# Kernel optimization log

Measured on AMD Instinct MI355X. Metric: run time of the kernel, lower is better.

Reference implementation:

```python
import jax, jax.numpy as jnp
import numpy as np

TAU = 2.0       # LIF time constant
VTH = 1.0       # V_THRESHOLD
ALPHA = 2.0     # ATan surrogate alpha (spikingjelly default)
SCALE = 0.125

@jax.custom_vjp
def spike(x):
    # Heaviside spike with ATan surrogate gradient
    return (x >= 0.0).astype(x.dtype)

def _spike_fwd(x):
    return (x >= 0.0).astype(x.dtype), x

def _spike_bwd(x, g):
    sg = (ALPHA / 2.0) / (1.0 + (jnp.pi / 2.0 * ALPHA * x) ** 2)
    return (g * sg,)

spike.defvjp(_spike_fwd, _spike_bwd)

def lif(x_seq):
    # multi-step LIF: v += (x - v)/tau; spike; hard reset (v_reset=0, detach_reset)
    def step(v, x):
        v = v + (x - v) / TAU
        s = spike(v - VTH)
        v = v * (1.0 - jax.lax.stop_gradient(s))
        return v, s
    _, s = jax.lax.scan(step, jnp.zeros_like(x_seq[0]), x_seq)
    return s

def conn_lif(x_seq, y_seq):
    # connecting LIF: membrane charged by conv output + identity shortcut
    def step(v, xy):
        x, y = xy
        v = v + ((x + y) - v) / TAU
        s = spike(v - VTH)
        v = v * (1.0 - jax.lax.stop_gradient(s))
        return v, s
    _, s = jax.lax.scan(step, jnp.zeros_like(x_seq[0]), (x_seq, y_seq))
    return s

def conv1x1(x, W, b):
    # x: [T,B,C,N]; 1x1 Conv1d == channel GEMM
    return jnp.einsum('tbcn,oc->tbon', x, W) + b[None, None, :, None]

def setup_inputs() -> dict:
    key = jax.random.key(0)
    T, B, C, H, W = 4, 16, 512, 32, 32
    ks = jax.random.split(key, 5)
    wscale = 1.0 / np.sqrt(C)
    inp = {
        'x': jax.random.normal(ks[0], (T, B, C, H, W), jnp.float32),
        'Wq': jax.random.normal(ks[1], (C, C), jnp.float32) * wscale,
        'bq': jnp.zeros((C,), jnp.float32),
        'Wk': jax.random.normal(ks[2], (C, C), jnp.float32) * wscale,
        'bk': jnp.zeros((C,), jnp.float32),
        'Wv': jax.random.normal(ks[3], (C, C), jnp.float32) * wscale,
        'bv': jnp.zeros((C,), jnp.float32),
        'Wp': jax.random.normal(ks[4], (C, C), jnp.float32) * wscale,
        'bp': jnp.zeros((C,), jnp.float32),
        'num_heads': 8,
    }
    return inp

def reference(x, Wq, bq, Wk, bk, Wv, bv, Wp, bp, num_heads):
    T, B, C, H, W = x.shape
    N = H * W
    h = num_heads
    d = C // h
    qkv_x = x.reshape(T, B, C, N)

    def to_heads(s):  # [T,B,C,N] -> [T,B,h,N,d]
        return s.reshape(T, B, h, d, N).transpose(0, 1, 2, 4, 3)

    q = to_heads(lif(conv1x1(qkv_x, Wq, bq)))
    k = to_heads(lif(conv1x1(qkv_x, Wk, bk)))
    v = to_heads(lif(conv1x1(qkv_x, Wv, bv)))

    kv = jnp.einsum('tbhnd,tbhne->tbhde', k, v)            # K^T V: [T,B,h,d,d]
    out = jnp.einsum('tbhnd,tbhde->tbhne', q, kv) * SCALE  # Q @ (K^T V)
    out = out.transpose(0, 1, 2, 4, 3).reshape(T, B, C, N)
    out = lif(out)                                          # attn_sn
    out = conv1x1(out, Wp, bp).reshape(T, B, C, H, W)       # proj_reparam
    out = conn_lif(out, x)                                  # proj_sn(out, x)
    return out
```

## Files before the change

kernel.cpp:

```cpp
#include <hip/hip_runtime.h>

#define T_ 4
#define B_ 16
#define C_ 512
#define N_ 1024
#define H_ 8
#define D_ 64
#define SPK_ELEMS (33554432ull)

typedef _Float16 half8v __attribute__((ext_vector_type(8)));
typedef _Float16 half4v __attribute__((ext_vector_type(4)));
typedef float f32x4 __attribute__((ext_vector_type(4)));

#define KV_OFF_N  100663296ull
#define WB_OFF_N  109051904ull
#define XS_OFF_N  113246208ull

#define QKV_INV_SCALE (1.0f / 8388608.0f)
#define PROJ_INV_SCALE (1.0f / 4096.0f)

#define GLD16(gp, loff) \
  __builtin_amdgcn_global_load_lds( \
      (const __attribute__((address_space(1))) void*)(gp), \
      (__attribute__((address_space(3))) void*)(lds + (loff)), 16, 0, 0)

__global__ __launch_bounds__(256) void convert_w(
    const float* __restrict__ w0, const float* __restrict__ w1,
    const float* __restrict__ w2, const float* __restrict__ w3,
    _Float16* __restrict__ wb)
{
  int idx = blockIdx.x * 256 + threadIdx.x;
  int p = idx >> 18, rem = idx & 262143;
  const float* src = (p == 0) ? w0 : (p == 1) ? w1 : (p == 2) ? w2 : w3;
  float v = src[rem] * 4096.0f;
  _Float16 h1 = (_Float16)v;
  float r1 = v - (float)h1;
  _Float16 h2 = (_Float16)r1;
  size_t base = ((size_t)(p * 2)) << 18;
  wb[base + rem] = h1;
  wb[base + 262144 + rem] = h2;
}

__global__ __launch_bounds__(256) void convert_x(
    const float* __restrict__ x, _Float16* __restrict__ xs)
{
  __shared__ float tile[32][33];
  const int tb = blockIdx.z;
  const int c0 = blockIdx.y * 32, n0 = blockIdx.x * 32;
  const int tx = threadIdx.x, ty = threadIdx.y;
  const float* src = x + ((size_t)tb * C_ + c0) * N_ + n0;
#pragma unroll
  for (int k = 0; k < 4; ++k)
    tile[ty + 8 * k][tx] = src[(size_t)(ty + 8 * k) * N_ + tx];
  __syncthreads();
#pragma unroll
  for (int k = 0; k < 4; ++k) {
    int r = ty + 8 * k;
    float v = tile[tx][r] * 2048.0f;
    _Float16 h1 = (_Float16)v;
    float r1 = v - (float)h1;
    _Float16 h2 = (_Float16)r1;
    size_t o = ((size_t)tb * N_ + n0 + r) * C_ + c0 + tx;
    xs[o] = h1;
    xs[o + 33554432ull] = h2;
  }
}

__global__ __launch_bounds__(512) void qkv_mfma(
    const _Float16* __restrict__ wb, const _Float16* __restrict__ xs,
    const float* __restrict__ bq, const float* __restrict__ bk,
    const float* __restrict__ bv, unsigned char* __restrict__ spikes_base)
{
  __shared__ __align__(16) char lds[81920];
  const int tid = threadIdx.x;
  const int lane = tid & 63, wave = tid >> 6;
  const int ln15 = lane & 15, lq = lane >> 4;
  const int wr = wave & 3, wn = wave >> 2;

  const int l = blockIdx.x + 12 * blockIdx.y + 384 * blockIdx.z;
  const int xcd = l & 7, slot = l >> 3;
  const int g = (slot / 12) * 8 + xcd;
  const int m = slot % 12;
  const int ot = m & 3, p = m >> 2;
  const int ntb = g & 31, b = g >> 5;
  const int o0 = ot * 128, n0 = ntb * 32;

#define WB_(k) (((k) & 1) * 16384)
#define XB_(k) (32768 + ((k) % 3) * 16384)

  const _Float16* gw[2];
#pragma unroll
  for (int i = 0; i < 2; ++i) {
    int u = i * 512 + tid;
    int s = u >> 9, rem = u & 511;
    int row = rem >> 2, pc = rem & 3;
    int lc = pc ^ ((row >> 1) & 3);
    gw[i] = wb + (((size_t)(p * 2 + s)) << 18) + (size_t)(o0 + row) * C_ + lc * 8;
  }
  const _Float16* gx[2];
#pragma unroll
  for (int i = 0; i < 2; ++i) {
    int v = i * 512 + tid;
    int s = v >> 9, rem = v & 511;
    int t = rem >> 7, rem2 = rem & 127;
    int row = rem2 >> 2, pc = rem2 & 3;
    int lc = pc ^ ((row >> 1) & 3);
    gx[i] = xs + ((size_t)s * 33554432ull) +
            ((size_t)((t * B_ + b) * N_ + n0 + row)) * C_ + lc * 8;
  }
  const int sb = (tid & 448) * 16;

  f32x4 acc[T_][2];
#pragma unroll
  for (int t = 0; t < T_; ++t)
#pragma unroll
    for (int mt = 0; mt < 2; ++mt)
      acc[t][mt] = (f32x4){0.f, 0.f, 0.f, 0.f};

  int offA[2][2], offB[2];
#pragma unroll
  for (int s = 0; s < 2; ++s) {
#pragma unroll
    for (int mt = 0; mt < 2; ++mt) {
      int r = wr * 32 + mt * 16 + ln15;
      offA[s][mt] = s * 8192 + r * 64 + ((lq ^ ((r >> 1) & 3)) << 4);
    }
    {
      int n = wn * 16 + ln15;
      offB[s] = s * 8192 + n * 64 + ((lq ^ ((n >> 1) & 3)) << 4);
    }
  }

  auto compute = [&](int wbase, int xbase) {
    half8v wa[2][2];
#pragma unroll
    for (int s = 0; s < 2; ++s)
#pragma unroll
      for (int mt = 0; mt < 2; ++mt)
        wa[s][mt] = *(const half8v*)&lds[wbase + offA[s][mt]];

    __builtin_amdgcn_s_setprio(1);
#pragma unroll
    for (int t = 0; t < T_; ++t) {
      half8v xb[2];
#pragma unroll
      for (int s = 0; s < 2; ++s)
        xb[s] = *(const half8v*)&lds[xbase + offB[s] + t * 2048];
#pragma unroll
      for (int mt = 0; mt < 2; ++mt) {
        f32x4 a = acc[t][mt];
        a = __builtin_amdgcn_mfma_f32_16x16x32_f16(wa[0][mt], xb[1], a, 0, 0, 0);
        a = __builtin_amdgcn_mfma_f32_16x16x32_f16(wa[1][mt], xb[0], a, 0, 0, 0);
        a = __builtin_amdgcn_mfma_f32_16x16x32_f16(wa[0][mt], xb[0], a, 0, 0, 0);
        acc[t][mt] = a;
      }
    }
    __builtin_amdgcn_s_setprio(0);
  };

#pragma unroll
  for (int i = 0; i < 2; ++i)
    GLD16(gx[i], XB_(0) + i * 8192 + sb);
#pragma unroll
  for (int i = 0; i < 2; ++i) gx[i] += 32;
#pragma unroll
  for (int i = 0; i < 2; ++i)
    GLD16(gw[i], WB_(0) + i * 8192 + sb);
#pragma unroll
  for (int i = 0; i < 2; ++i) gw[i] += 32;
#pragma unroll
  for (int i = 0; i < 2; ++i)
    GLD16(gx[i], XB_(1) + i * 8192 + sb);
#pragma unroll
  for (int i = 0; i < 2; ++i) gx[i] += 32;
  asm volatile("s_waitcnt vmcnt(2)" ::: "memory");
  __builtin_amdgcn_s_barrier();
  __builtin_amdgcn_sched_barrier(0);

#pragma unroll
  for (int kk = 0; kk < 16; ++kk) {
    if (kk < 15) {
#pragma unroll
      for (int i = 0; i < 2; ++i)
        GLD16(gw[i], WB_(kk + 1) + i * 8192 + sb);
#pragma unroll
      for (int i = 0; i < 2; ++i) gw[i] += 32;
    }
    if (kk < 14) {
#pragma unroll
      for (int i = 0; i < 2; ++i)
        GLD16(gx[i], XB_(kk + 2) + i * 8192 + sb);
#pragma unroll
      for (int i = 0; i < 2; ++i) gx[i] += 32;
    }
    __builtin_amdgcn_sched_barrier(0);

    compute(WB_(kk), XB_(kk));

    if (kk < 15) {
      __builtin_amdgcn_sched_barrier(0);
      if (kk < 14) asm volatile("s_waitcnt vmcnt(2)" ::: "memory");
      else         asm volatile("s_waitcnt vmcnt(0)" ::: "memory");
      __builtin_amdgcn_s_barrier();
      __builtin_amdgcn_sched_barrier(0);
    }
  }

#undef WB_
#undef XB_

  const float* bias = (p == 0) ? bq : (p == 1) ? bk : bv;
  const int n = n0 + wn * 16 + ln15;
  if (p == 0) {
    unsigned char* spq = spikes_base;
#pragma unroll
    for (int mt = 0; mt < 2; ++mt) {
      int obase = o0 + wr * 32 + mt * 16 + lq * 4;
      float b4[4] = {bias[obase], bias[obase + 1], bias[obase + 2], bias[obase + 3]};
      float vm[4] = {0.f, 0.f, 0.f, 0.f};
#pragma unroll
      for (int t = 0; t < T_; ++t) {
        unsigned char sj[4];
#pragma unroll
        for (int r = 0; r < 4; ++r) {
          float y = acc[t][mt][r] * QKV_INV_SCALE + b4[r];
          float v = vm[r] + (y - vm[r]) * 0.5f;
          bool s = (v >= 1.0f);
          sj[r] = s ? 1 : 0;
          vm[r] = s ? 0.f : v;
        }
        *(uchar4*)&spq[((size_t)(t * B_ + b) * N_ + n) * C_ + obase] =
            make_uchar4(sj[0], sj[1], sj[2], sj[3]);
      }
    }
  } else {
    unsigned char* sp = spikes_base + (size_t)p * SPK_ELEMS;
#pragma unroll
    for (int mt = 0; mt < 2; ++mt)
#pragma unroll
      for (int r = 0; r < 4; ++r) {
        int o = o0 + wr * 32 + mt * 16 + lq * 4 + r;
        float bo = bias[o];
        float vmem = 0.f;
#pragma unroll
        for (int t = 0; t < T_; ++t) {
          float y = acc[t][mt][r] * QKV_INV_SCALE + bo;
          float v = vmem + (y - vmem) * 0.5f;
          bool s = (v >= 1.0f);
          sp[((size_t)(t * B_ + b) * C_ + o) * N_ + n] = s ? 1 : 0;
          vmem = s ? 0.f : v;
        }
      }
  }
}

__global__ __launch_bounds__(256) void kv_f16(
    const unsigned char* __restrict__ sk, const unsigned char* __restrict__ sv,
    float* __restrict__ kvout)
{
  __shared__ _Float16 Kf[64 * 264];
  __shared__ _Float16 Vf[64 * 264];
  const int tid = threadIdx.x;
  const int lane = tid & 63, wave = tid >> 6;
  const int ln15 = lane & 15, lq = lane >> 4;
  const int h = blockIdx.x, b = blockIdx.y, t = blockIdx.z;

  const unsigned char* kb = sk + ((size_t)(t * B_ + b) * C_ + h * D_) * N_;
  const unsigned char* vb = sv + ((size_t)(t * B_ + b) * C_ + h * D_) * N_;

  f32x4 acc[4];
#pragma unroll
  for (int et = 0; et < 4; ++et) acc[et] = (f32x4){0.f, 0.f, 0.f, 0.f};

  const int row = tid >> 2, seg = (tid & 3) * 64;

  for (int nc = 0; nc < N_; nc += 256) {
    const unsigned char* kr = kb + (size_t)row * N_ + nc + seg;
    const unsigned char* vr = vb + (size_t)row * N_ + nc + seg;
#pragma unroll
    for (int j = 0; j < 16; ++j) {
      unsigned wk = *(const unsigned*)(kr + j * 4);
      unsigned lo = ((wk & 0xFFu) | ((wk & 0xFF00u) << 8)) * 0x3C00u;
      unsigned hi = (((wk >> 16) & 0xFFu) | ((wk >> 8) & 0xFF0000u)) * 0x3C00u;
      *(uint2*)&Kf[row * 264 + seg + j * 4] = make_uint2(lo, hi);
      unsigned wv = *(const unsigned*)(vr + j * 4);
      unsigned lo2 = ((wv & 0xFFu) | ((wv & 0xFF00u) << 8)) * 0x3C00u;
      unsigned hi2 = (((wv >> 16) & 0xFFu) | ((wv >> 8) & 0xFF0000u)) * 0x3C00u;
      *(uint2*)&Vf[row * 264 + seg + j * 4] = make_uint2(lo2, hi2);
    }
    __syncthreads();
#pragma unroll
    for (int ks = 0; ks < 8; ++ks) {
      half8v a = *(const half8v*)&Kf[(wave * 16 + ln15) * 264 + ks * 32 + lq * 8];
#pragma unroll
      for (int et = 0; et < 4; ++et) {
        half8v bf = *(const half8v*)&Vf[(et * 16 + ln15) * 264 + ks * 32 + lq * 8];
        acc[et] = __builtin_amdgcn_mfma_f32_16x16x32_f16(a, bf, acc[et], 0, 0, 0);
      }
    }
    __syncthreads();
  }

  float* o = kvout + ((size_t)(t * B_ + b) * H_ + h) * (D_ * D_);
#pragma unroll
  for (int et = 0; et < 4; ++et)
#pragma unroll
    for (int r = 0; r < 4; ++r) {
      int d = wave * 16 + lq * 4 + r;
      int e = et * 16 + ln15;
      o[d * D_ + e] = acc[et][r];
    }
}

__global__ __launch_bounds__(256) void attn_mfma(
    const unsigned char* __restrict__ sq2, const float* __restrict__ kv,
    unsigned short* __restrict__ sa)
{
  __shared__ _Float16 Qs[128 * 72];
  __shared__ _Float16 KVT[64 * 72];
  const int tid = threadIdx.x;
  const int lane = tid & 63, wave = tid >> 6;
  const int ln15 = lane & 15, lq = lane >> 4;
  const int n0 = blockIdx.x * 128;
  const int h = blockIdx.y, b = blockIdx.z;

  f32x4 vm[8];
#pragma unroll
  for (int nt = 0; nt < 8; ++nt) vm[nt] = (f32x4){0.f, 0.f, 0.f, 0.f};

  for (int t = 0; t < T_; ++t) {
    __syncthreads();
    const float* kvb = kv + ((size_t)(t * B_ + b) * H_ + h) * (D_ * D_);
#pragma unroll
    for (int l = 0; l < 16; ++l) {
      int idx = l * 256 + tid;
      int e = idx & 63, d = idx >> 6;
      KVT[e * 72 + d] = (_Float16)kvb[d * 64 + e];
    }
    const unsigned char* qb = sq2 + ((size_t)(t * B_ + b) * N_ + n0) * C_ + h * D_;
#pragma unroll
    for (int l = 0; l < 8; ++l) {
      int idx = l * 256 + tid;
      int n = idx >> 4, d4 = (idx & 15) * 4;
      uchar4 qu = *(const uchar4*)&qb[(size_t)n * C_ + d4];
      half4v hv;
      hv.x = qu.x ? (_Float16)1.0f : (_Float16)0.0f;
      hv.y = qu.y ? (_Float16)1.0f : (_Float16)0.0f;
      hv.z = qu.z ? (_Float16)1.0f : (_Float16)0.0f;
      hv.w = qu.w ? (_Float16)1.0f : (_Float16)0.0f;
      *(half4v*)&Qs[n * 72 + d4] = hv;
    }
    __syncthreads();

    half8v af[2];
#pragma unroll
    for (int kk = 0; kk < 2; ++kk)
      af[kk] = *(const half8v*)&KVT[(wave * 16 + ln15) * 72 + kk * 32 + lq * 8];

#pragma unroll
    for (int nt = 0; nt < 8; ++nt) {
      f32x4 a = (f32x4){0.f, 0.f, 0.f, 0.f};
#pragma unroll
      for (int kk = 0; kk < 2; ++kk) {
        half8v bf = *(const half8v*)&Qs[(nt * 16 + ln15) * 72 + kk * 32 + lq * 8];
        a = __builtin_amdgcn_mfma_f32_16x16x32_f16(af[kk], bf, a, 0, 0, 0);
      }
      unsigned short sj[4];
#pragma unroll
      for (int r = 0; r < 4; ++r) {
        float y = a[r] * 0.125f;
        float v = vm[nt][r] + (y - vm[nt][r]) * 0.5f;
        bool s = (v >= 1.0f);
        sj[r] = s ? 0x3C00 : 0;
        vm[nt][r] = s ? 0.f : v;
      }
      int n = n0 + nt * 16 + ln15;
      int c0 = h * D_ + wave * 16 + lq * 4;
      *(ushort4*)&sa[((size_t)(t * B_ + b) * N_ + n) * C_ + c0] =
          make_ushort4(sj[0], sj[1], sj[2], sj[3]);
    }
  }
}

__global__ __launch_bounds__(256) void proj_mfma(
    const _Float16* __restrict__ wb, const _Float16* __restrict__ sa,
    const float* __restrict__ bp, const float* __restrict__ x,
    float* __restrict__ out)
{
  __shared__ __align__(16) char lds[49152];
  const int tid = threadIdx.x;
  const int lane = tid & 63, wave = tid >> 6;
  const int ln15 = lane & 15, lq = lane >> 4;

  const int l = blockIdx.x + 4 * blockIdx.y + 128 * blockIdx.z;
  const int xcd = l & 7, slot = l >> 3;
  const int g = (slot / 4) * 8 + xcd;
  const int ot = slot % 4;
  const int ntb = g & 31, b = g >> 5;
  const int o0 = ot * 128, n0 = ntb * 32;

  const _Float16* gsrc[6];
#pragma unroll
  for (int i = 0; i < 6; ++i) {
    int u = i * 256 + tid;
    if (u < 1024) {
      int s = u >> 9, rem = u & 511;
      int row = rem >> 2, pc = rem & 3;
      int lc = pc ^ ((row >> 1) & 3);
      gsrc[i] = wb + (((size_t)(3 * 2 + s)) << 18) + (size_t)(o0 + row) * C_ + lc * 8;
    } else {
      int v = u - 1024;
      int t = v >> 7, rem2 = v & 127;
      int row = rem2 >> 2, pc = rem2 & 3;
      int lc = pc ^ ((row >> 1) & 3);
      gsrc[i] = sa + ((size_t)((t * B_ + b) * N_ + n0 + row)) * C_ + lc * 8;
    }
  }

  f32x4 acc[T_][2][2];
#pragma unroll
  for (int t = 0; t < T_; ++t)
#pragma unroll
    for (int mt = 0; mt < 2; ++mt)
#pragma unroll
      for (int nt = 0; nt < 2; ++nt)
        acc[t][mt][nt] = (f32x4){0.f, 0.f, 0.f, 0.f};

  int offA[2][2], offB[2];
#pragma unroll
  for (int s = 0; s < 2; ++s)
#pragma unroll
    for (int mt = 0; mt < 2; ++mt) {
      int r = wave * 32 + mt * 16 + ln15;
      offA[s][mt] = s * 8192 + r * 64 + ((lq ^ ((r >> 1) & 3)) << 4);
    }
#pragma unroll
  for (int nt = 0; nt < 2; ++nt) {
    int n = nt * 16 + ln15;
    offB[nt] = 16384 + n * 64 + ((lq ^ ((n >> 1) & 3)) << 4);
  }

  auto compute = [&](int cur) {
    half8v wa[2][2];
#pragma unroll
    for (int s = 0; s < 2; ++s)
#pragma unroll
      for (int mt = 0; mt < 2; ++mt)
        wa[s][mt] = *(const half8v*)&lds[cur + offA[s][mt]];

    __builtin_amdgcn_s_setprio(1);
#pragma unroll
    for (int t = 0; t < T_; ++t) {
      half8v xb[2];
#pragma unroll
      for (int nt = 0; nt < 2; ++nt)
        xb[nt] = *(const half8v*)&lds[cur + offB[nt] + t * 2048];
#pragma unroll
      for (int mt = 0; mt < 2; ++mt)
#pragma unroll
        for (int nt = 0; nt < 2; ++nt) {
          f32x4 a = acc[t][mt][nt];
          a = __builtin_amdgcn_mfma_f32_16x16x32_f16(wa[1][mt], xb[nt], a, 0, 0, 0);
          a = __builtin_amdgcn_mfma_f32_16x16x32_f16(wa[0][mt], xb[nt], a, 0, 0, 0);
          acc[t][mt][nt] = a;
        }
    }
    __builtin_amdgcn_s_setprio(0);
  };

#pragma unroll
  for (int i = 0; i < 6; ++i)
    GLD16(gsrc[i], i * 4096 + (tid & 192) * 16);
#pragma unroll
  for (int i = 0; i < 6; ++i) gsrc[i] += 32;

  for (int kk = 0; kk < 15; ++kk) {
    const int cur = (kk & 1) * 24576;
    const int nxt = 24576 - cur;
#pragma unroll
    for (int i = 0; i < 6; ++i)
      GLD16(gsrc[i], nxt + i * 4096 + (tid & 192) * 16);
#pragma unroll
    for (int i = 0; i < 6; ++i) gsrc[i] += 32;
    __builtin_amdgcn_sched_barrier(0);
    asm volatile("s_waitcnt vmcnt(6)" ::: "memory");
    __builtin_amdgcn_s_barrier();
    __builtin_amdgcn_sched_barrier(0);

    compute(cur);

    asm volatile("s_waitcnt lgkmcnt(0)" ::: "memory");
    __builtin_amdgcn_sched_barrier(0);
    __builtin_amdgcn_s_barrier();
  }
  asm volatile("s_waitcnt vmcnt(0)" ::: "memory");
  __builtin_amdgcn_s_barrier();
  __builtin_amdgcn_sched_barrier(0);
  compute(24576);

#pragma unroll
  for (int mt = 0; mt < 2; ++mt)
#pragma unroll
    for (int r = 0; r < 4; ++r) {
      int o = o0 + wave * 32 + mt * 16 + lq * 4 + r;
      float bo = bp[o];
#pragma unroll
      for (int nt = 0; nt < 2; ++nt) {
        int n = n0 + nt * 16 + ln15;
        float vmem = 0.f;
#pragma unroll
        for (int t = 0; t < T_; ++t) {
          size_t base = ((size_t)(t * B_ + b) * C_ + o) * N_ + n;
          float xv = x[base];
          float pv = acc[t][mt][nt][r] * PROJ_INV_SCALE + bo;
          float v = vmem + ((pv + xv) - vmem) * 0.5f;
          bool s = (v >= 1.0f);
          out[base] = s ? 1.0f : 0.0f;
          vmem = s ? 0.f : v;
        }
      }
    }
}

extern "C" void kernel_launch(void* const* d_in, const int* in_sizes, int n_in,
                              void* d_out, int out_size, void* d_ws, size_t ws_size,
                              hipStream_t stream)
{
  const float* x  = (const float*)d_in[0];
  const float* Wq = (const float*)d_in[1];
  const float* bq = (const float*)d_in[2];
  const float* Wk = (const float*)d_in[3];
  const float* bk = (const float*)d_in[4];
  const float* Wv = (const float*)d_in[5];
  const float* bv = (const float*)d_in[6];
  const float* Wp = (const float*)d_in[7];
  const float* bp = (const float*)d_in[8];
  (void)in_sizes; (void)n_in; (void)out_size; (void)ws_size;

  unsigned char* ws = (unsigned char*)d_ws;
  unsigned char* sq = ws;
  unsigned char* sk = ws + SPK_ELEMS;
  unsigned char* sv = ws + 2 * SPK_ELEMS;
  float* kvbuf = (float*)(ws + KV_OFF_N);
  _Float16* wb = (_Float16*)(ws + WB_OFF_N);
  _Float16* xs = (_Float16*)(ws + XS_OFF_N);
  unsigned short* sa = (unsigned short*)xs;
  float* out = (float*)d_out;

  convert_w<<<4096, 256, 0, stream>>>(Wq, Wk, Wv, Wp, wb);
  convert_x<<<dim3(32, 16, 64), dim3(32, 8), 0, stream>>>(x, xs);
  qkv_mfma<<<dim3(12, 32, 16), 512, 0, stream>>>(wb, xs, bq, bk, bv, ws);
  kv_f16<<<dim3(8, 16, 4), 256, 0, stream>>>(sk, sv, kvbuf);
  attn_mfma<<<dim3(8, 8, 16), 256, 0, stream>>>(sq, kvbuf, sa);
  proj_mfma<<<dim3(4, 32, 16), 256, 0, stream>>>(wb, (const _Float16*)sa, bp, x, out);
}
```

Baseline: 748.2 us.

## Vectorize convert_x transpose and rework proj_mfma into 512-thread triple-buffered pipeline

convert_x now uses 64x64 tiles with float4 global loads and half4 vector stores in place of scalar accesses, which cuts the number of memory transactions in the transpose. proj_mfma moves from 4 to 8 waves per block, giving each wave a 16-column N slice. Weight tiles are now double-buffered and spike tiles triple-buffered, with a prefetch depth of two for spikes. The aim is better latency hiding and higher occupancy in the projection GEMM, at the cost of more LDS per block and more complex wait counts.

```diff
diff --git a/kernel.cpp b/kernel.cpp
--- a/kernel.cpp
+++ b/kernel.cpp
@@ -44,25 +44,42 @@
 __global__ __launch_bounds__(256) void convert_x(
     const float* __restrict__ x, _Float16* __restrict__ xs)
 {
-  __shared__ float tile[32][33];
+  __shared__ float tile[64][65];
   const int tb = blockIdx.z;
-  const int c0 = blockIdx.y * 32, n0 = blockIdx.x * 32;
-  const int tx = threadIdx.x, ty = threadIdx.y;
-  const float* src = x + ((size_t)tb * C_ + c0) * N_ + n0;
-#pragma unroll
-  for (int k = 0; k < 4; ++k)
-    tile[ty + 8 * k][tx] = src[(size_t)(ty + 8 * k) * N_ + tx];
+  const int c0 = blockIdx.y * 64, n0 = blockIdx.x * 64;
+  const int tid = threadIdx.x;
+  {
+    const int tx = tid & 15, ty = tid >> 4;
+    const float* src = x + ((size_t)tb * C_ + c0 + ty) * N_ + n0 + tx * 4;
+#pragma unroll
+    for (int k = 0; k < 4; ++k) {
+      float4 v = *(const float4*)(src + (size_t)(16 * k) * N_);
+      tile[ty + 16 * k][tx * 4 + 0] = v.x;
+      tile[ty + 16 * k][tx * 4 + 1] = v.y;
+      tile[ty + 16 * k][tx * 4 + 2] = v.z;
+      tile[ty + 16 * k][tx * 4 + 3] = v.w;
+    }
+  }
   __syncthreads();
-#pragma unroll
-  for (int k = 0; k < 4; ++k) {
-    int r = ty + 8 * k;
-    float v = tile[tx][r] * 2048.0f;
-    _Float16 h1 = (_Float16)v;
-    float r1 = v - (float)h1;
-    _Float16 h2 = (_Float16)r1;
-    size_t o = ((size_t)tb * N_ + n0 + r) * C_ + c0 + tx;
-    xs[o] = h1;
-    xs[o + 33554432ull] = h2;
+  {
+    const int cg = tid & 15, nl = tid >> 4;
+#pragma unroll
+    for (int k = 0; k < 4; ++k) {
+      int n = nl + 16 * k;
+      half4v d0, d1;
+#pragma unroll
+      for (int j = 0; j < 4; ++j) {
+        float v = tile[cg * 4 + j][n] * 2048.0f;
+        _Float16 h1 = (_Float16)v;
+        float r1 = v - (float)h1;
+        _Float16 h2 = (_Float16)r1;
+        d0[j] = h1;
+        d1[j] = h2;
+      }
+      size_t o = ((size_t)tb * N_ + n0 + n) * C_ + c0 + cg * 4;
+      *(half4v*)&xs[o] = d0;
+      *(half4v*)&xs[o + 33554432ull] = d1;
+    }
   }
 }
 
@@ -382,15 +399,16 @@
   }
 }
 
-__global__ __launch_bounds__(256) void proj_mfma(
+__global__ __launch_bounds__(512) void proj_mfma(
     const _Float16* __restrict__ wb, const _Float16* __restrict__ sa,
     const float* __restrict__ bp, const float* __restrict__ x,
     float* __restrict__ out)
 {
-  __shared__ __align__(16) char lds[49152];
+  __shared__ __align__(16) char lds[57344];
   const int tid = threadIdx.x;
   const int lane = tid & 63, wave = tid >> 6;
   const int ln15 = lane & 15, lq = lane >> 4;
+  const int wr = wave & 3, wn = wave >> 2;
 
   const int l = blockIdx.x + 4 * blockIdx.y + 128 * blockIdx.z;
   const int xcd = l & 7, slot = l >> 3;
@@ -399,125 +417,129 @@
   const int ntb = g & 31, b = g >> 5;
   const int o0 = ot * 128, n0 = ntb * 32;
 
-  const _Float16* gsrc[6];
-#pragma unroll
-  for (int i = 0; i < 6; ++i) {
-    int u = i * 256 + tid;
-    if (u < 1024) {
-      int s = u >> 9, rem = u & 511;
-      int row = rem >> 2, pc = rem & 3;
-      int lc = pc ^ ((row >> 1) & 3);
-      gsrc[i] = wb + (((size_t)(3 * 2 + s)) << 18) + (size_t)(o0 + row) * C_ + lc * 8;
-    } else {
-      int v = u - 1024;
-      int t = v >> 7, rem2 = v & 127;
-      int row = rem2 >> 2, pc = rem2 & 3;
-      int lc = pc ^ ((row >> 1) & 3);
-      gsrc[i] = sa + ((size_t)((t * B_ + b) * N_ + n0 + row)) * C_ + lc * 8;
-    }
-  }
-
-  f32x4 acc[T_][2][2];
+#define WB_(k) (((k) & 1) * 16384)
+#define SB_(k) (32768 + ((k) % 3) * 8192)
+
+  const _Float16* gw[2];
+#pragma unroll
+  for (int i = 0; i < 2; ++i) {
+    int u = i * 512 + tid;
+    int s = u >> 9, rem = u & 511;
+    int row = rem >> 2, pc = rem & 3;
+    int lc = pc ^ ((row >> 1) & 3);
+    gw[i] = wb + (((size_t)(3 * 2 + s)) << 18) + (size_t)(o0 + row) * C_ + lc * 8;
+  }
+  const _Float16* gs;
+  {
+    int t = tid >> 7, rem2 = tid & 127;
+    int row = rem2 >> 2, pc = rem2 & 3;
+    int lc = pc ^ ((row >> 1) & 3);
+    gs = sa + ((size_t)((t * B_ + b) * N_ + n0 + row)) * C_ + lc * 8;
+  }
+  const int sb = (tid & 448) * 16;
+
+  f32x4 acc[T_][2];
 #pragma unroll
   for (int t = 0; t < T_; ++t)
 #pragma unroll
     for (int mt = 0; mt < 2; ++mt)
-#pragma unroll
-      for (int nt = 0; nt < 2; ++nt)
-        acc[t][mt][nt] = (f32x4){0.f, 0.f, 0.f, 0.f};
-
-  int offA[2][2], offB[2];
+      acc[t][mt] = (f32x4){0.f, 0.f, 0.f, 0.f};
+
+  int offA[2][2], offB;
 #pragma unroll
   for (int s = 0; s < 2; ++s)
 #pragma unroll
     for (int mt = 0; mt < 2; ++mt) {
-      int r = wave * 32 + mt * 16 + ln15;
+      int r = wr * 32 + mt * 16 + ln15;
       offA[s][mt] = s * 8192 + r * 64 + ((lq ^ ((r >> 1) & 3)) << 4);
     }
-#pragma unroll
-  for (int nt = 0; nt < 2; ++nt) {
-    int n = nt * 16 + ln15;
-    offB[nt] = 16384 + n * 64 + ((lq ^ ((n >> 1) & 3)) << 4);
-  }
-
-  auto compute = [&](int cur) {
+  {
+    int n = wn * 16 + ln15;
+    offB = n * 64 + ((lq ^ ((n >> 1) & 3)) << 4);
+  }
+
+  auto compute = [&](int wbase, int sbase) {
     half8v wa[2][2];
 #pragma unroll
     for (int s = 0; s < 2; ++s)
 #pragma unroll
       for (int mt = 0; mt < 2; ++mt)
-        wa[s][mt] = *(const half8v*)&lds[cur + offA[s][mt]];
+        wa[s][mt] = *(const half8v*)&lds[wbase + offA[s][mt]];
 
     __builtin_amdgcn_s_setprio(1);
 #pragma unroll
     for (int t = 0; t < T_; ++t) {
-      half8v xb[2];
-#pragma unroll
-      for (int nt = 0; nt < 2; ++nt)
-        xb[nt] = *(const half8v*)&lds[cur + offB[nt] + t * 2048];
-#pragma unroll
-      for (int mt = 0; mt < 2; ++mt)
-#pragma unroll
-        for (int nt = 0; nt < 2; ++nt) {
-          f32x4 a = acc[t][mt][nt];
-          a = __builtin_amdgcn_mfma_f32_16x16x32_f16(wa[1][mt], xb[nt], a, 0, 0, 0);
-          a = __builtin_amdgcn_mfma_f32_16x16x32_f16(wa[0][mt], xb[nt], a, 0, 0, 0);
-          acc[t][mt][nt] = a;
-        }
+      half8v xb = *(const half8v*)&lds[sbase + offB + t * 2048];
+#pragma unroll
+      for (int mt = 0; mt < 2; ++mt) {
+        f32x4 a = acc[t][mt];
+        a = __builtin_amdgcn_mfma_f32_16x16x32_f16(wa[1][mt], xb, a, 0, 0, 0);
+        a = __builtin_amdgcn_mfma_f32_16x16x32_f16(wa[0][mt], xb, a, 0, 0, 0);
+        acc[t][mt] = a;
+      }
     }
     __builtin_amdgcn_s_setprio(0);
   };
 
-#pragma unroll
-  for (int i = 0; i < 6; ++i)
-    GLD16(gsrc[i], i * 4096 + (tid & 192) * 16);
-#pragma unroll
-  for (int i = 0; i < 6; ++i) gsrc[i] += 32;
-
-  for (int kk = 0; kk < 15; ++kk) {
-    const int cur = (kk & 1) * 24576;
-    const int nxt = 24576 - cur;
-#pragma unroll
-    for (int i = 0; i < 6; ++i)
-      GLD16(gsrc[i], nxt + i * 4096 + (tid & 192) * 16);
-#pragma unroll
-    for (int i = 0; i < 6; ++i) gsrc[i] += 32;
-    __builtin_amdgcn_sched_barrier(0);
-    asm volatile("s_waitcnt vmcnt(6)" ::: "memory");
-    __builtin_amdgcn_s_barrier();
-    __builtin_amdgcn_sched_barrier(0);
-
-    compute(cur);
-
-    asm volatile("s_waitcnt lgkmcnt(0)" ::: "memory");
-    __builtin_amdgcn_sched_barrier(0);
-    __builtin_amdgcn_s_barrier();
-  }
-  asm volatile("s_waitcnt vmcnt(0)" ::: "memory");
+  GLD16(gs, SB_(0) + sb);
+  gs += 32;
+#pragma unroll
+  for (int i = 0; i < 2; ++i)
+    GLD16(gw[i], WB_(0) + i * 8192 + sb);
+#pragma unroll
+  for (int i = 0; i < 2; ++i) gw[i] += 32;
+  GLD16(gs, SB_(1) + sb);
+  gs += 32;
+  asm volatile("s_waitcnt vmcnt(1)" ::: "memory");
   __builtin_amdgcn_s_barrier();
   __builtin_amdgcn_sched_barrier(0);
-  compute(24576);
-
+
+#pragma unroll
+  for (int kk = 0; kk < 16; ++kk) {
+    if (kk < 15) {
+#pragma unroll
+      for (int i = 0; i < 2; ++i)
+        GLD16(gw[i], WB_(kk + 1) + i * 8192 + sb);
+#pragma unroll
+      for (int i = 0; i < 2; ++i) gw[i] += 32;
+    }
+    if (kk < 14) {
+      GLD16(gs, SB_(kk + 2) + sb);
+      gs += 32;
+    }
+    __builtin_amdgcn_sched_barrier(0);
+
+    compute(WB_(kk), SB_(kk));
+
+    if (kk < 15) {
+      __builtin_amdgcn_sched_barrier(0);
+      if (kk < 14) asm volatile("s_waitcnt vmcnt(1)" ::: "memory");
+      else         asm volatile("s_waitcnt vmcnt(0)" ::: "memory");
+      __builtin_amdgcn_s_barrier();
+      __builtin_amdgcn_sched_barrier(0);
+    }
+  }
+
+#undef WB_
+#undef SB_
+
+  const int n = n0 + wn * 16 + ln15;
 #pragma unroll
   for (int mt = 0; mt < 2; ++mt)
 #pragma unroll
     for (int r = 0; r < 4; ++r) {
-      int o = o0 + wave * 32 + mt * 16 + lq * 4 + r;
+      int o = o0 + wr * 32 + mt * 16 + lq * 4 + r;
       float bo = bp[o];
-#pragma unroll
-      for (int nt = 0; nt < 2; ++nt) {
-        int n = n0 + nt * 16 + ln15;
-        float vmem = 0.f;
-#pragma unroll
-        for (int t = 0; t < T_; ++t) {
-          size_t base = ((size_t)(t * B_ + b) * C_ + o) * N_ + n;
-          float xv = x[base];
-          float pv = acc[t][mt][nt][r] * PROJ_INV_SCALE + bo;
-          float v = vmem + ((pv + xv) - vmem) * 0.5f;
-          bool s = (v >= 1.0f);
-          out[base] = s ? 1.0f : 0.0f;
-          vmem = s ? 0.f : v;
-        }
+      float vmem = 0.f;
+#pragma unroll
+      for (int t = 0; t < T_; ++t) {
+        size_t base = ((size_t)(t * B_ + b) * C_ + o) * N_ + n;
+        float xv = x[base];
+        float pv = acc[t][mt][r] * PROJ_INV_SCALE + bo;
+        float v = vmem + ((pv + xv) - vmem) * 0.5f;
+        bool s = (v >= 1.0f);
+        out[base] = s ? 1.0f : 0.0f;
+        vmem = s ? 0.f : v;
       }
     }
 }
@@ -548,9 +570,9 @@
   float* out = (float*)d_out;
 
   convert_w<<<4096, 256, 0, stream>>>(Wq, Wk, Wv, Wp, wb);
-  convert_x<<<dim3(32, 16, 64), dim3(32, 8), 0, stream>>>(x, xs);
+  convert_x<<<dim3(16, 8, 64), 256, 0, stream>>>(x, xs);
   qkv_mfma<<<dim3(12, 32, 16), 512, 0, stream>>>(wb, xs, bq, bk, bv, ws);
   kv_f16<<<dim3(8, 16, 4), 256, 0, stream>>>(sk, sv, kvbuf);
   attn_mfma<<<dim3(8, 8, 16), 256, 0, stream>>>(sq, kvbuf, sa);
-  proj_mfma<<<dim3(4, 32, 16), 256, 0, stream>>>(wb, (const _Float16*)sa, bp, x, out);
-}
+  proj_mfma<<<dim3(4, 32, 16), 512, 0, stream>>>(wb, (const _Float16*)sa, bp, x, out);
+}
```

After: 763.8 us. 2.1% more time.
